# Kernel optimization log

Hardware: AMD Instinct MI355X
Metric: run time of the kernel (lower is better)

The kernel has to match this reference:

```python
import jax, jax.numpy as jnp
import numpy as np

ANCHORS = np.array([116., 90., 156., 198., 373., 326.], np.float32).reshape(1, 1, 1, 3, 2)
IGNORE_THRESH = 0.5
OBJ_SCALE = 5.0
NOOBJ_SCALE = 1.0
XYWH_SCALE = 1.0
CLASS_SCALE = 1.0
GRID_SCALE = 1.0


def setup_inputs() -> dict:
    key = jax.random.key(0)
    k1, k2, k3 = jax.random.split(key, 3)
    B, GH, GW, NET, T, C = 16, 64, 64, 1024, 100, 80
    input_image = jnp.zeros((B, NET, NET, 3), jnp.float32)  # only shape is used
    y_pred = jax.random.normal(k1, (B, GH, GW, 3 * (5 + C)), jnp.float32)
    y_true = jax.random.uniform(k2, (B, GH, GW, 3, 5 + C), jnp.float32)
    true_boxes = jax.random.uniform(k3, (B, 1, 1, 1, T, 4), jnp.float32)
    return {"input_image": input_image, "y_pred": y_pred, "y_true": y_true, "true_boxes": true_boxes}


def reference(input_image, y_pred, y_true, true_boxes):
    B, GH, GW = y_true.shape[:3]
    net_h, net_w = input_image.shape[1], input_image.shape[2]
    dtype = y_pred.dtype
    anchors = jnp.asarray(ANCHORS, dtype)  # [1,1,1,3,2]
    y_pred = y_pred.reshape(B, GH, GW, 3, -1)
    object_mask = y_true[..., 4:5]  # [B,GH,GW,3,1]
    grid_factor = jnp.array([GW, GH], dtype).reshape(1, 1, 1, 1, 2)
    net_factor = jnp.array([net_w, net_h], dtype).reshape(1, 1, 1, 1, 2)
    cx, cy = jnp.meshgrid(jnp.arange(GW, dtype=dtype), jnp.arange(GH, dtype=dtype))
    cell_grid = jnp.stack([cx, cy], -1)[None, :, :, None, :]  # [1,GH,GW,1,2]

    # adjust predictions
    pred_box_xy = cell_grid + jax.nn.sigmoid(y_pred[..., :2])
    pred_box_wh = y_pred[..., 2:4]
    pred_box_conf = jax.nn.sigmoid(y_pred[..., 4:5])
    pred_box_class = y_pred[..., 5:]

    # adjust ground truth
    true_box_xy = y_true[..., 0:2]
    true_box_wh = y_true[..., 2:4]
    true_box_class = jnp.argmax(y_true[..., 5:], axis=-1)  # [B,GH,GW,3]

    # broadcast IoU: each predicted box vs all true boxes
    true_xy = true_boxes[..., 0:2] / grid_factor  # [B,1,1,1,T,2]
    true_wh = true_boxes[..., 2:4] / net_factor
    true_half = true_wh / 2.0
    true_mins, true_maxes = true_xy - true_half, true_xy + true_half
    pred_xy = (pred_box_xy / grid_factor)[..., None, :]  # [B,GH,GW,3,1,2]
    pred_wh = (jnp.exp(pred_box_wh) * anchors / net_factor)[..., None, :]
    pred_half = pred_wh / 2.0
    pred_mins, pred_maxes = pred_xy - pred_half, pred_xy + pred_half
    inter_wh = jnp.maximum(jnp.minimum(pred_maxes, true_maxes) - jnp.maximum(pred_mins, true_mins), 0.0)
    inter_area = inter_wh[..., 0] * inter_wh[..., 1]  # [B,GH,GW,3,T]
    true_area = true_wh[..., 0] * true_wh[..., 1]
    pred_area = pred_wh[..., 0] * pred_wh[..., 1]
    iou = inter_area / (pred_area + true_area - inter_area)
    best_ious = jnp.max(iou, axis=4)
    conf_ignore_mask = (best_ious > IGNORE_THRESH).astype(dtype)[..., None]

    # post-warmup branch (batch_seen > warmup_batches)
    xywh_mask = object_mask

    wh_scale = jnp.exp(true_box_wh) * anchors / net_factor
    wh_scale = (2.0 - wh_scale[..., 0] * wh_scale[..., 1])[..., None]

    xy_delta = xywh_mask * (true_box_xy - pred_box_xy) * wh_scale * XYWH_SCALE
    wh_delta = xywh_mask * (true_box_wh - pred_box_wh) * wh_scale * XYWH_SCALE
    conf_delta = (0.0 - pred_box_conf) * NOOBJ_SCALE
    conf_delta = conf_delta + object_mask * (1.0 - pred_box_conf) * OBJ_SCALE
    conf_delta = conf_delta * (1.0 - (1.0 - object_mask) * conf_ignore_mask)
    log_p = jax.nn.log_softmax(pred_box_class, axis=-1)
    ce = -jnp.take_along_axis(log_p, true_box_class[..., None], axis=-1)  # [B,GH,GW,3,1]
    class_delta = object_mask * ce * CLASS_SCALE

    delta = jnp.concatenate([xy_delta, wh_delta, conf_delta, class_delta], axis=-1)  # [B,GH,GW,3,6]
    loss = jnp.sum(jnp.square(delta), axis=(1, 2, 3, 4))
    return loss * GRID_SCALE
```

## Files before the change

### kernel.cpp

```cpp
#include <hip/hip_runtime.h>


#define NC 80
#define NT 100
#define CPB 12288
#define NTOT 196608

typedef float f4 __attribute__((ext_vector_type(4)));
typedef f4 f4a __attribute__((aligned(4)));

__device__ __forceinline__ float frcp(float x) { return __builtin_amdgcn_rcpf(x); }
__device__ __forceinline__ float fsig(float x) { return frcp(1.f + __expf(-x)); }

__global__ __launch_bounds__(256, 4) void yolo_loss_kernel(
    const float* __restrict__ y_pred,
    const float* __restrict__ y_true,
    const float* __restrict__ true_boxes,
    float* __restrict__ out)
{
    __shared__ f4 sbox[NT];
    __shared__ float swsum[4];

    const int tid = threadIdx.x;
    const int idx = blockIdx.x * 256 + tid;
    const int b   = idx / CPB;

    if (tid < NT) {
        const f4 tb = *(const f4*)(true_boxes + (size_t)b * NT * 4 + tid * 4);
        const float tx = tb.x * (1.f / 64.f),   ty = tb.y * (1.f / 64.f);
        const float tw = tb.z * (1.f / 1024.f), th = tb.w * (1.f / 1024.f);
        f4 r;
        r.x = tx - 0.5f * tw; r.y = ty - 0.5f * th;
        r.z = tx + 0.5f * tw; r.w = ty + 0.5f * th;
        sbox[tid] = r;
    }
    __syncthreads();

    const int rem = idx % CPB;
    const int gy  = rem / 192;
    const int rr  = rem - gy * 192;
    const int gx  = rr / 3;
    const int a   = rr - gx * 3;
    const float aw = (a == 0) ? 116.f : ((a == 1) ? 156.f : 373.f);
    const float ah = (a == 0) ? 90.f  : ((a == 1) ? 198.f : 326.f);

    const float* p = y_pred + (size_t)idx * 85;
    const float* t = y_true + (size_t)idx * 85;

    const f4 ph = *(const f4a*)p;   const float p4v = p[4];
    const f4 th = *(const f4a*)t;   const float om  = t[4];

    const f4a* pc4 = (const f4a*)(p + 5);
    const f4a* tc4 = (const f4a*)(t + 5);

    float ssum = 0.f;
    float tmax = -1e30f, psel = 0.f;

    f4 pa[4], ta[4];
#pragma unroll
    for (int k = 0; k < 4; ++k) { pa[k] = pc4[k]; ta[k] = tc4[k]; }

#pragma unroll
    for (int bch = 0; bch < 5; ++bch) {
        f4 pb[4], tb[4];
#pragma unroll
        for (int k = 0; k < 4; ++k) { pb[k] = pa[k]; tb[k] = ta[k]; }
        if (bch < 4) {
#pragma unroll
            for (int k = 0; k < 4; ++k) {
                pa[k] = pc4[(bch + 1) * 4 + k];
                ta[k] = tc4[(bch + 1) * 4 + k];
            }
        }
#pragma unroll
        for (int k = 0; k < 4; ++k) {
#pragma unroll
            for (int c = 0; c < 4; ++c) {
                const float pv = pb[k][c];
                const float tv = tb[k][c];
                ssum += __expf(pv);
                const bool g = tv > tmax;
                tmax = g ? tv : tmax;
                psel = g ? pv : psel;
            }
        }
    }
    const float ce = __logf(ssum) - psel;

    const float predx = (float)gx + fsig(ph.x);
    const float predy = (float)gy + fsig(ph.y);
    const float conf  = fsig(p4v);
    const float pw = __expf(ph.z) * aw * (1.f / 1024.f);
    const float phh = __expf(ph.w) * ah * (1.f / 1024.f);
    const float parea = pw * phh;
    const float px = predx * (1.f / 64.f), py = predy * (1.f / 64.f);
    const float pminx = px - 0.5f * pw,  pmaxx = px + 0.5f * pw;
    const float pminy = py - 0.5f * phh, pmaxy = py + 0.5f * phh;

    float best = 0.f;
#pragma unroll 4
    for (int ti = 0; ti < NT; ++ti) {
        const f4 bx = sbox[ti];
        float iw = fminf(pmaxx, bx.z) - fmaxf(pminx, bx.x);
        float ih = fminf(pmaxy, bx.w) - fmaxf(pminy, bx.y);
        iw = fmaxf(iw, 0.f); ih = fmaxf(ih, 0.f);
        const float inter = iw * ih;
        const float tarea = (bx.z - bx.x) * (bx.w - bx.y);
        best = fmaxf(best, inter * frcp(parea + tarea - inter));
    }
    const float ignore = (best > 0.5f) ? 1.f : 0.f;

    const float wsx = __expf(th.z) * aw * (1.f / 1024.f);
    const float wsy = __expf(th.w) * ah * (1.f / 1024.f);
    const float ws  = 2.f - wsx * wsy;
    const float omws = om * ws;
    const float dx = omws * (th.x - predx);
    const float dy = omws * (th.y - predy);
    const float dw = omws * (th.z - ph.z);
    const float dh = omws * (th.w - ph.w);
    float dc = -conf + om * (1.f - conf) * 5.f;
    dc *= (1.f - (1.f - om) * ignore);
    const float dcl = om * ce;

    float val = dx * dx + dy * dy + dw * dw + dh * dh + dc * dc + dcl * dcl;

#pragma unroll
    for (int off = 32; off > 0; off >>= 1) val += __shfl_down(val, off, 64);
    if ((tid & 63) == 0) swsum[tid >> 6] = val;
    __syncthreads();
    if (tid == 0) atomicAdd(out + b, swsum[0] + swsum[1] + swsum[2] + swsum[3]);
}

extern "C" void kernel_launch(void* const* d_in, const int* in_sizes, int n_in,
                              void* d_out, int out_size, void* d_ws, size_t ws_size,
                              hipStream_t stream) {
    const float* y_pred     = (const float*)d_in[1];
    const float* y_true     = (const float*)d_in[2];
    const float* true_boxes = (const float*)d_in[3];
    float* out = (float*)d_out;

    hipMemsetAsync(d_out, 0, (size_t)out_size * sizeof(float), stream);
    yolo_loss_kernel<<<NTOT / 256, 256, 0, stream>>>(y_pred, y_true, true_boxes, out);
}
```

Measured before the change: 366.4 us.

## Split each anchor row across two threads for class scan and IoU loop

Each anchor row is now handled by a pair of threads. Each thread scans half of the 80 class logits and half of the 100 true boxes, and the pair combines sum-exp, argmax and best IoU through xor shuffles. This doubles the number of threads so more loads are in flight and per-thread latency drops, at the cost of repeating the header loads and box math in both threads and adding shuffle overhead. Launch bounds are relaxed from 4 to 2 waves per SIMD.

```diff
diff --git a/kernel.cpp b/kernel.cpp
--- a/kernel.cpp
+++ b/kernel.cpp
@@ -1,7 +1,6 @@
 #include <hip/hip_runtime.h>
 
 
-#define NC 80
 #define NT 100
 #define CPB 12288
 #define NTOT 196608
@@ -12,7 +11,7 @@
 __device__ __forceinline__ float frcp(float x) { return __builtin_amdgcn_rcpf(x); }
 __device__ __forceinline__ float fsig(float x) { return frcp(1.f + __expf(-x)); }
 
-__global__ __launch_bounds__(256, 4) void yolo_loss_kernel(
+__global__ __launch_bounds__(256, 2) void yolo_loss_kernel(
     const float* __restrict__ y_pred,
     const float* __restrict__ y_true,
     const float* __restrict__ true_boxes,
@@ -22,8 +21,10 @@
     __shared__ float swsum[4];
 
     const int tid = threadIdx.x;
-    const int idx = blockIdx.x * 256 + tid;
-    const int b   = idx / CPB;
+    const int gth = blockIdx.x * 256 + tid;
+    const int row = gth >> 1;
+    const int q   = gth & 1;
+    const int b   = row / CPB;
 
     if (tid < NT) {
         const f4 tb = *(const f4*)(true_boxes + (size_t)b * NT * 4 + tid * 4);
@@ -36,7 +37,7 @@
     }
     __syncthreads();
 
-    const int rem = idx % CPB;
+    const int rem = row % CPB;
     const int gy  = rem / 192;
     const int rr  = rem - gy * 192;
     const int gx  = rr / 3;
@@ -44,53 +45,49 @@
     const float aw = (a == 0) ? 116.f : ((a == 1) ? 156.f : 373.f);
     const float ah = (a == 0) ? 90.f  : ((a == 1) ? 198.f : 326.f);
 
-    const float* p = y_pred + (size_t)idx * 85;
-    const float* t = y_true + (size_t)idx * 85;
+    const float* p = y_pred + (size_t)row * 85;
+    const float* t = y_true + (size_t)row * 85;
 
     const f4 ph = *(const f4a*)p;   const float p4v = p[4];
     const f4 th = *(const f4a*)t;   const float om  = t[4];
 
-    const f4a* pc4 = (const f4a*)(p + 5);
-    const f4a* tc4 = (const f4a*)(t + 5);
+    const f4a* pc4 = (const f4a*)(p + 5 + 40 * q);
+    const f4a* tc4 = (const f4a*)(t + 5 + 40 * q);
 
     float ssum = 0.f;
     float tmax = -1e30f, psel = 0.f;
 
-    f4 pa[4], ta[4];
-#pragma unroll
-    for (int k = 0; k < 4; ++k) { pa[k] = pc4[k]; ta[k] = tc4[k]; }
-
+    f4 pa0 = pc4[0], pa1 = pc4[1], ta0 = tc4[0], ta1 = tc4[1];
 #pragma unroll
     for (int bch = 0; bch < 5; ++bch) {
-        f4 pb[4], tb[4];
-#pragma unroll
-        for (int k = 0; k < 4; ++k) { pb[k] = pa[k]; tb[k] = ta[k]; }
+        const f4 pb0 = pa0, pb1 = pa1, tb0 = ta0, tb1 = ta1;
         if (bch < 4) {
-#pragma unroll
-            for (int k = 0; k < 4; ++k) {
-                pa[k] = pc4[(bch + 1) * 4 + k];
-                ta[k] = tc4[(bch + 1) * 4 + k];
-            }
+            pa0 = pc4[2 * bch + 2]; pa1 = pc4[2 * bch + 3];
+            ta0 = tc4[2 * bch + 2]; ta1 = tc4[2 * bch + 3];
         }
 #pragma unroll
-        for (int k = 0; k < 4; ++k) {
-#pragma unroll
-            for (int c = 0; c < 4; ++c) {
-                const float pv = pb[k][c];
-                const float tv = tb[k][c];
-                ssum += __expf(pv);
-                const bool g = tv > tmax;
-                tmax = g ? tv : tmax;
-                psel = g ? pv : psel;
-            }
+        for (int c = 0; c < 4; ++c) {
+            float pv = pb0[c], tv = tb0[c];
+            ssum += __expf(pv);
+            bool g = tv > tmax;
+            tmax = g ? tv : tmax; psel = g ? pv : psel;
+            pv = pb1[c]; tv = tb1[c];
+            ssum += __expf(pv);
+            g = tv > tmax;
+            tmax = g ? tv : tmax; psel = g ? pv : psel;
         }
     }
+    ssum += __shfl_xor(ssum, 1, 64);
+    const float otmax = __shfl_xor(tmax, 1, 64);
+    const float opsel = __shfl_xor(psel, 1, 64);
+    const bool adopt = (otmax > tmax) || (otmax == tmax && q == 1);
+    psel = adopt ? opsel : psel;
     const float ce = __logf(ssum) - psel;
 
     const float predx = (float)gx + fsig(ph.x);
     const float predy = (float)gy + fsig(ph.y);
     const float conf  = fsig(p4v);
-    const float pw = __expf(ph.z) * aw * (1.f / 1024.f);
+    const float pw  = __expf(ph.z) * aw * (1.f / 1024.f);
     const float phh = __expf(ph.w) * ah * (1.f / 1024.f);
     const float parea = pw * phh;
     const float px = predx * (1.f / 64.f), py = predy * (1.f / 64.f);
@@ -98,8 +95,8 @@
     const float pminy = py - 0.5f * phh, pmaxy = py + 0.5f * phh;
 
     float best = 0.f;
-#pragma unroll 4
-    for (int ti = 0; ti < NT; ++ti) {
+#pragma unroll 5
+    for (int ti = q; ti < NT; ti += 2) {
         const f4 bx = sbox[ti];
         float iw = fminf(pmaxx, bx.z) - fmaxf(pminx, bx.x);
         float ih = fminf(pmaxy, bx.w) - fmaxf(pminy, bx.y);
@@ -108,6 +105,7 @@
         const float tarea = (bx.z - bx.x) * (bx.w - bx.y);
         best = fmaxf(best, inter * frcp(parea + tarea - inter));
     }
+    best = fmaxf(best, __shfl_xor(best, 1, 64));
     const float ignore = (best > 0.5f) ? 1.f : 0.f;
 
     const float wsx = __expf(th.z) * aw * (1.f / 1024.f);
@@ -123,6 +121,7 @@
     const float dcl = om * ce;
 
     float val = dx * dx + dy * dy + dw * dw + dh * dh + dc * dc + dcl * dcl;
+    val = (q == 0) ? val : 0.f;
 
 #pragma unroll
     for (int off = 32; off > 0; off >>= 1) val += __shfl_down(val, off, 64);
@@ -140,5 +139,5 @@
     float* out = (float*)d_out;
 
     hipMemsetAsync(d_out, 0, (size_t)out_size * sizeof(float), stream);
-    yolo_loss_kernel<<<NTOT / 256, 256, 0, stream>>>(y_pred, y_true, true_boxes, out);
+    yolo_loss_kernel<<<(NTOT * 2) / 256, 256, 0, stream>>>(y_pred, y_true, true_boxes, out);
 }
```

New measurement: 328.3 us. -10.4%, faster.
